# Optimization experiments

Measured on AMD Instinct MI355X. Metric: run time of the kernel, lower is better.

## Reference

```python
import jax, jax.numpy as jnp
import numpy as np

B, S, E, H = 4, 1024, 1024, 16
HD = E // H  # 64


def setup_inputs() -> dict:
    key = jax.random.key(0)
    ks = jax.random.split(key, 9)
    scale = 1.0 / np.sqrt(E)
    x = jax.random.normal(ks[0], (B, S, E), dtype=jnp.float32)
    attention_mask = jnp.ones((B, S, S), dtype=jnp.int32)
    # per-head projection weights, batched over heads: [H, E, HD]
    Wq = jax.random.normal(ks[1], (H, E, HD), dtype=jnp.float32) * scale
    Wk = jax.random.normal(ks[2], (H, E, HD), dtype=jnp.float32) * scale
    Wv = jax.random.normal(ks[3], (H, E, HD), dtype=jnp.float32) * scale
    bq = jax.random.normal(ks[4], (H, HD), dtype=jnp.float32) * scale
    bk = jax.random.normal(ks[5], (H, HD), dtype=jnp.float32) * scale
    bv = jax.random.normal(ks[6], (H, HD), dtype=jnp.float32) * scale
    # output projection, torch Linear convention: [out_features, in_features]
    Wo = jax.random.normal(ks[7], (E, E), dtype=jnp.float32) * scale
    bo = jax.random.normal(ks[8], (E,), dtype=jnp.float32) * scale
    return {"x": x, "attention_mask": attention_mask, "Wq": Wq, "bq": bq,
            "Wk": Wk, "bk": bk, "Wv": Wv, "bv": bv, "Wo": Wo, "bo": bo}


def reference(x, attention_mask, Wq, bq, Wk, bk, Wv, bv, Wo, bo):
    # batched-over-heads QKV projections: (B,S,E) x (H,E,HD) -> (B,H,S,HD)
    q = jnp.einsum('bse,hed->bhsd', x, Wq) + bq[None, :, None, :]
    k = jnp.einsum('bse,hed->bhsd', x, Wk) + bk[None, :, None, :]
    v = jnp.einsum('bse,hed->bhsd', x, Wv) + bv[None, :, None, :]
    scores = jnp.einsum('bhsd,bhtd->bhst', q, k) / jnp.sqrt(jnp.float32(HD))
    mask = attention_mask[:, None, :, :]  # (B,1,S,S) broadcast over heads
    scores = jnp.where(mask == 0, -jnp.inf, scores)
    weights = jax.nn.softmax(scores, axis=-1)
    out = jnp.einsum('bhst,bhtd->bhsd', weights, v)
    # concat heads on last dim: (B,S,H*HD) == (B,S,E)
    out = out.transpose(0, 2, 1, 3).reshape(B, S, E)
    return out @ Wo.T + bo
```

## Files before the change

### kernel.cpp

```cpp
#include <hip/hip_runtime.h>
#include <hip/hip_bf16.h>

#define NB 4
#define SEQ 1024
#define EMB 1024
#define NH 16
#define HD 64

typedef unsigned short u16;
typedef __attribute__((ext_vector_type(8))) __bf16 bf16x8;
typedef __attribute__((ext_vector_type(8))) short short8;
typedef __attribute__((ext_vector_type(4))) float floatx4;

__device__ inline u16 f2b_rn(float f) {
    union { float f; unsigned int i; } x; x.f = f;
    unsigned int r = (x.i + 0x7FFFu + ((x.i >> 16) & 1u)) >> 16;
    return (u16)r;
}
__device__ inline bf16x8 s2b(short8 v) {
    union { short8 s; bf16x8 b; } x; x.s = v; return x.b;
}

__device__ inline void gload_lds16(const void* g, void* l) {
    __builtin_amdgcn_global_load_lds(
        (const __attribute__((address_space(1))) void*)g,
        (__attribute__((address_space(3))) void*)l, 16, 0, 0);
}

__device__ inline bf16x8 ldsfrag(const u16* base, int r, int c) {
    return s2b(*(const short8*)&base[r * 64 + (c ^ ((r & 7) * 8))]);
}

__device__ inline void cvt8(const float* __restrict__ s, u16* __restrict__ d) {
    float4 a = *(const float4*)(s);
    float4 b = *(const float4*)(s + 4);
    union { u16 u[8]; int4 v; } o;
    o.u[0] = f2b_rn(a.x); o.u[1] = f2b_rn(a.y); o.u[2] = f2b_rn(a.z); o.u[3] = f2b_rn(a.w);
    o.u[4] = f2b_rn(b.x); o.u[5] = f2b_rn(b.y); o.u[6] = f2b_rn(b.z); o.u[7] = f2b_rn(b.w);
    *(int4*)(d) = o.v;
}

__global__ __launch_bounds__(256) void prep(
    const float* __restrict__ x, const float* __restrict__ Wq,
    const float* __restrict__ Wk, const float* __restrict__ Wv,
    const float* __restrict__ Wo, const int* __restrict__ mask,
    u16* __restrict__ xb, u16* __restrict__ Wt, u16* __restrict__ Wob,
    unsigned long long* __restrict__ bits)
{
    __shared__ u16 T[64 * 80];
    int bx = blockIdx.x;
    int tid = threadIdx.x;

    if (bx < 2048) {
        int i = bx * 2048 + tid * 8;
        cvt8(x + i, xb + i);
    } else if (bx < 2560) {
        int i = (bx - 2048) * 2048 + tid * 8;
        cvt8(Wo + i, Wob + i);
    } else if (bx < 3328) {
        int bx2 = bx - 2560;
        int e0 = (bx2 & 15) * 64;
        int ph = bx2 >> 4;
        int p = ph >> 4, h = ph & 15;
        const float* W = (p == 0 ? Wq : (p == 1 ? Wk : Wv)) + h * (EMB * HD);
        #pragma unroll
        for (int c = 0; c < 2; ++c) {
            int flat = c * 2048 + tid * 8;
            int r = flat >> 6;
            int d = flat & 63;
            cvt8(W + (size_t)(e0 + r) * HD + d, &T[r * 80 + d]);
        }
        __syncthreads();
        int d = tid >> 2;
        int ec = tid & 3;
        union { u16 u[16]; int4 v[2]; } tmp;
        #pragma unroll
        for (int i = 0; i < 16; ++i) tmp.u[i] = T[(ec * 16 + i) * 80 + d];
        u16* dst = Wt + ((size_t)(p * NH + h) * HD + d) * EMB + e0 + ec * 16;
        *(int4*)(dst) = tmp.v[0];
        *(int4*)(dst + 8) = tmp.v[1];
    } else {
        int gw = (bx - 3328) * 4 + (tid >> 6);
        int lane = tid & 63;
        int m = mask[(size_t)gw * 64 + lane];
        unsigned long long bl = __ballot(m != 0);
        if (lane == 0) bits[gw] = bl;
    }
}

__global__ __launch_bounds__(256) void qkv_gemm(
    const u16* __restrict__ x,
    const u16* __restrict__ Wt2,
    const float* __restrict__ bq, const float* __restrict__ bk, const float* __restrict__ bv,
    u16* __restrict__ Q, u16* __restrict__ K, u16* __restrict__ Vt)
{
    __shared__ u16 As[128 * 64];
    __shared__ u16 Bs[128 * 64];

    int m0 = blockIdx.x * 128;
    int n0 = blockIdx.y * 128;
    int tid = threadIdx.x;
    int w = tid >> 6, lane = tid & 63, quad = lane >> 4, ln = lane & 15;
    int wm = w & 1, wn = w >> 1;

    floatx4 acc[4][4] = {};

    for (int k0 = 0; k0 < EMB; k0 += 64) {
        __syncthreads();
        #pragma unroll
        for (int i = 0; i < 4; ++i) {
            int flat0 = i * 256 + (tid & 192);
            int flat = flat0 + lane;
            int r = flat >> 3;
            int c = ((flat & 7) ^ (r & 7)) * 8;
            gload_lds16(x   + (size_t)(m0 + r) * EMB + k0 + c, As + flat0 * 8);
            gload_lds16(Wt2 + (size_t)(n0 + r) * EMB + k0 + c, Bs + flat0 * 8);
        }
        __syncthreads();

        #pragma unroll
        for (int kk = 0; kk < 2; ++kk) {
            bf16x8 a[4], bf[4];
            #pragma unroll
            for (int mt = 0; mt < 4; ++mt)
                a[mt] = ldsfrag(As, wm * 64 + mt * 16 + ln, kk * 32 + quad * 8);
            #pragma unroll
            for (int nc = 0; nc < 4; ++nc)
                bf[nc] = ldsfrag(Bs, wn * 64 + nc * 16 + ln, kk * 32 + quad * 8);
            #pragma unroll
            for (int mt = 0; mt < 4; ++mt)
                #pragma unroll
                for (int nc = 0; nc < 4; ++nc)
                    acc[mt][nc] = __builtin_amdgcn_mfma_f32_16x16x32_bf16(a[mt], bf[nc], acc[mt][nc], 0, 0, 0);
        }
    }

    int p = n0 >> 10;
    const float* bias = (p == 0 ? bq : (p == 1 ? bk : bv));
    if (p < 2) {
        u16* Out = (p == 0) ? Q : K;
        float qs = (p == 0) ? 0.125f * 1.44269504f : 1.0f;
        #pragma unroll
        for (int nc = 0; nc < 4; ++nc) {
            int n = n0 + wn * 64 + nc * 16 + ln;
            int h = (n >> 6) & 15, d = n & 63;
            float bv_ = bias[n & 1023];
            #pragma unroll
            for (int mt = 0; mt < 4; ++mt) {
                #pragma unroll
                for (int reg = 0; reg < 4; ++reg) {
                    int m = m0 + wm * 64 + mt * 16 + quad * 4 + reg;
                    int b_ = m >> 10, s = m & 1023;
                    Out[((size_t)(b_ * NH + h) * SEQ + s) * HD + d] = f2b_rn((acc[mt][nc][reg] + bv_) * qs);
                }
            }
        }
    } else {
        #pragma unroll
        for (int nc = 0; nc < 4; ++nc) {
            int n = n0 + wn * 64 + nc * 16 + ln;
            int h = (n >> 6) & 15, d = n & 63;
            float bv_ = bias[n & 1023];
            #pragma unroll
            for (int mt = 0; mt < 4; ++mt) {
                int m = m0 + wm * 64 + mt * 16 + quad * 4;
                int b_ = m >> 10, s = m & 1023;
                union { u16 u[4]; uint2 v; } pk;
                #pragma unroll
                for (int reg = 0; reg < 4; ++reg)
                    pk.u[reg] = f2b_rn(acc[mt][nc][reg] + bv_);
                *(uint2*)&Vt[((size_t)(b_ * NH + h) * HD + d) * SEQ + s] = pk.v;
            }
        }
    }
}

__global__ __launch_bounds__(128) void attn(
    const u16* __restrict__ Q, const u16* __restrict__ K, const u16* __restrict__ Vt,
    const unsigned long long* __restrict__ bits,
    u16* __restrict__ Aout)
{
    const int PP = 72;
    __shared__ u16 Ks[64 * 64];
    __shared__ u16 Vs[80 * 64];
    __shared__ u16 Ps[64 * PP];

    int q0 = blockIdx.x * 64;
    int bh = blockIdx.y;
    int b = bh >> 4, h = bh & 15;
    const u16* Qb = Q  + (size_t)bh * SEQ * HD;
    const u16* Kb = K  + (size_t)bh * SEQ * HD;
    const u16* Vb = Vt + (size_t)bh * HD * SEQ;

    int tid = threadIdx.x;
    int w = tid >> 6, lane = tid & 63, quad = lane >> 4, ln = lane & 15;

    if (tid < 16) *(uint2*)&Vs[64 * 64 + tid * 4] = make_uint2(0x3F803F80u, 0x3F803F80u);

    bf16x8 qf[2][2];
    #pragma unroll
    for (int s = 0; s < 2; ++s) {
        const u16* qp = Qb + (size_t)(q0 + w * 32 + s * 16 + ln) * HD + quad * 8;
        union { int4 i; bf16x8 b; } c0, c1;
        c0.i = *(const int4*)(qp);
        c1.i = *(const int4*)(qp + 32);
        qf[s][0] = c0.b; qf[s][1] = c1.b;
    }

    floatx4 o[2][5] = {};

    for (int tt = 0; tt < SEQ / 64; ++tt) {
        int t0 = tt * 64;
        __syncthreads();
        #pragma unroll
        for (int i = 0; i < 4; ++i) {
            int flat0 = i * 128 + (tid & 64);
            int flat = flat0 + lane;
            int r = flat >> 3;
            int c = ((flat & 7) ^ (r & 7)) * 8;
            gload_lds16(Kb + (size_t)(t0 + r) * HD + c, Ks + flat0 * 8);
            gload_lds16(Vb + (size_t)r * SEQ + t0 + c, Vs + flat0 * 8);
        }
        __syncthreads();

        floatx4 sc[2][4] = {};
        #pragma unroll
        for (int kk = 0; kk < 2; ++kk) {
            bf16x8 kf[4];
            #pragma unroll
            for (int tb = 0; tb < 4; ++tb)
                kf[tb] = ldsfrag(Ks, tb * 16 + ln, kk * 32 + quad * 8);
            #pragma unroll
            for (int s = 0; s < 2; ++s)
                #pragma unroll
                for (int tb = 0; tb < 4; ++tb)
                    sc[s][tb] = __builtin_amdgcn_mfma_f32_16x16x32_bf16(kf[tb], qf[s][kk], sc[s][tb], 0, 0, 0);
        }

        #pragma unroll
        for (int s = 0; s < 2; ++s) {
            unsigned long long bm = bits[((size_t)b * SEQ + q0 + w * 32 + s * 16 + ln) * 16 + tt];
            if (__any(bm != ~0ull)) {
                #pragma unroll
                for (int tb = 0; tb < 4; ++tb)
                    #pragma unroll
                    for (int reg = 0; reg < 4; ++reg)
                        if (!((bm >> (tb * 16 + quad * 4 + reg)) & 1)) sc[s][tb][reg] = -1e30f;
            }
        }

        #pragma unroll
        for (int s = 0; s < 2; ++s) {
            int mrow = w * 32 + s * 16 + ln;
            #pragma unroll
            for (int tb = 0; tb < 4; ++tb) {
                union { float f; unsigned int i; } e0_, e1_, e2_, e3_;
                e0_.f = __builtin_amdgcn_exp2f(sc[s][tb][0]);
                e1_.f = __builtin_amdgcn_exp2f(sc[s][tb][1]);
                e2_.f = __builtin_amdgcn_exp2f(sc[s][tb][2]);
                e3_.f = __builtin_amdgcn_exp2f(sc[s][tb][3]);
                uint2 pk;
                pk.x = ((e0_.i + 0x8000u) >> 16) | ((e1_.i + 0x8000u) & 0xFFFF0000u);
                pk.y = ((e2_.i + 0x8000u) >> 16) | ((e3_.i + 0x8000u) & 0xFFFF0000u);
                *(uint2*)&Ps[mrow * PP + tb * 16 + quad * 4] = pk;
            }
        }

        #pragma unroll
        for (int kk = 0; kk < 2; ++kk) {
            bf16x8 vf[5];
            #pragma unroll
            for (int dt = 0; dt < 5; ++dt)
                vf[dt] = ldsfrag(Vs, dt * 16 + ln, kk * 32 + quad * 8);
            #pragma unroll
            for (int s = 0; s < 2; ++s) {
                bf16x8 pf = s2b(*(const short8*)&Ps[(w * 32 + s * 16 + ln) * PP + kk * 32 + quad * 8]);
                #pragma unroll
                for (int dt = 0; dt < 5; ++dt)
                    o[s][dt] = __builtin_amdgcn_mfma_f32_16x16x32_bf16(pf, vf[dt], o[s][dt], 0, 0, 0);
            }
        }
    }

    #pragma unroll
    for (int s = 0; s < 2; ++s) {
        #pragma unroll
        for (int reg = 0; reg < 4; ++reg) {
            float l = __shfl(o[s][4][reg], lane & 48, 64);
            float inv = 1.0f / l;
            int m = q0 + w * 32 + s * 16 + quad * 4 + reg;
            #pragma unroll
            for (int dt = 0; dt < 4; ++dt)
                Aout[((size_t)b * SEQ + m) * EMB + h * HD + dt * 16 + ln] = f2b_rn(o[s][dt][reg] * inv);
        }
    }
}

__global__ __launch_bounds__(256) void out_proj(
    const u16* __restrict__ A,
    const u16* __restrict__ Wo,
    const float* __restrict__ bo,
    float* __restrict__ Out)
{
    __shared__ u16 As[128 * 64];
    __shared__ u16 Bs[128 * 64];

    int m0 = blockIdx.x * 128;
    int n0 = blockIdx.y * 128;
    int tid = threadIdx.x;
    int w = tid >> 6, lane = tid & 63, quad = lane >> 4, ln = lane & 15;
    int wm = w & 1, wn = w >> 1;

    floatx4 acc[4][4] = {};

    for (int k0 = 0; k0 < EMB; k0 += 64) {
        __syncthreads();
        #pragma unroll
        for (int i = 0; i < 4; ++i) {
            int flat0 = i * 256 + (tid & 192);
            int flat = flat0 + lane;
            int r = flat >> 3;
            int c = ((flat & 7) ^ (r & 7)) * 8;
            gload_lds16(A  + (size_t)(m0 + r) * EMB + k0 + c, As + flat0 * 8);
            gload_lds16(Wo + (size_t)(n0 + r) * EMB + k0 + c, Bs + flat0 * 8);
        }
        __syncthreads();

        #pragma unroll
        for (int kk = 0; kk < 2; ++kk) {
            bf16x8 a[4], bf[4];
            #pragma unroll
            for (int mt = 0; mt < 4; ++mt)
                a[mt] = ldsfrag(As, wm * 64 + mt * 16 + ln, kk * 32 + quad * 8);
            #pragma unroll
            for (int nc = 0; nc < 4; ++nc)
                bf[nc] = ldsfrag(Bs, wn * 64 + nc * 16 + ln, kk * 32 + quad * 8);
            #pragma unroll
            for (int mt = 0; mt < 4; ++mt)
                #pragma unroll
                for (int nc = 0; nc < 4; ++nc)
                    acc[mt][nc] = __builtin_amdgcn_mfma_f32_16x16x32_bf16(a[mt], bf[nc], acc[mt][nc], 0, 0, 0);
        }
    }

    #pragma unroll
    for (int nc = 0; nc < 4; ++nc) {
        int n = n0 + wn * 64 + nc * 16 + ln;
        float bb = bo[n];
        #pragma unroll
        for (int mt = 0; mt < 4; ++mt) {
            #pragma unroll
            for (int reg = 0; reg < 4; ++reg) {
                int m = m0 + wm * 64 + mt * 16 + quad * 4 + reg;
                Out[(size_t)m * EMB + n] = acc[mt][nc][reg] + bb;
            }
        }
    }
}

extern "C" void kernel_launch(void* const* d_in, const int* in_sizes, int n_in,
                              void* d_out, int out_size, void* d_ws, size_t ws_size,
                              hipStream_t stream) {
    const float* x  = (const float*)d_in[0];
    const int*   mk = (const int*)d_in[1];
    const float* Wq = (const float*)d_in[2];
    const float* bq = (const float*)d_in[3];
    const float* Wk = (const float*)d_in[4];
    const float* bk = (const float*)d_in[5];
    const float* Wv = (const float*)d_in[6];
    const float* bv = (const float*)d_in[7];
    const float* Wo = (const float*)d_in[8];
    const float* bo = (const float*)d_in[9];
    float* out = (float*)d_out;

    const size_t MB = 1u << 20;
    char* ws = (char*)d_ws;
    u16* xb  = (u16*)ws;
    u16* Wt  = (u16*)(ws + 8 * MB);
    u16* Wob = (u16*)(ws + 14 * MB);
    unsigned long long* bits = (unsigned long long*)(ws + 16 * MB);
    u16* Qw  = (u16*)(ws + 16 * MB + 512 * 1024);
    u16* Kw  = (u16*)(ws + 24 * MB + 512 * 1024);
    u16* Vtw = (u16*)(ws + 32 * MB + 512 * 1024);
    u16* Ao  = xb;

    prep<<<19712, 256, 0, stream>>>(x, Wq, Wk, Wv, Wo, mk, xb, Wt, Wob, bits);
    qkv_gemm<<<dim3((NB * SEQ) / 128, 3 * EMB / 128), 256, 0, stream>>>(
        xb, Wt, bq, bk, bv, Qw, Kw, Vtw);
    attn<<<dim3(SEQ / 64, NB * NH), 128, 0, stream>>>(Qw, Kw, Vtw, bits, Ao);
    out_proj<<<dim3((NB * SEQ) / 128, EMB / 128), 256, 0, stream>>>(Ao, Wob, bo, out);
}
```

Before: 207.7 us.

## Rebalance work across prep, attention and output projection kernels

The mask-to-bitmask pass now has each wave process 16 rows, which cuts the prep grid size. Attention blocks go from 2 to 4 waves, each owning 16 query rows instead of 32. This lowers per-thread registers and splits K/V tile loading across more threads. The output projection halves its M tile to 64, doubling the grid to give better CU coverage at the cost of more B-tile reloads per output.

```diff
diff --git a/kernel.cpp b/kernel.cpp
--- a/kernel.cpp
+++ b/kernel.cpp
@@ -80,11 +80,15 @@
         *(int4*)(dst) = tmp.v[0];
         *(int4*)(dst + 8) = tmp.v[1];
     } else {
-        int gw = (bx - 3328) * 4 + (tid >> 6);
+        int base = (bx - 3328) * 64 + (tid >> 6) * 16;
         int lane = tid & 63;
-        int m = mask[(size_t)gw * 64 + lane];
-        unsigned long long bl = __ballot(m != 0);
-        if (lane == 0) bits[gw] = bl;
+        #pragma unroll
+        for (int i = 0; i < 16; ++i) {
+            int gw = base + i;
+            int m = mask[(size_t)gw * 64 + lane];
+            unsigned long long bl = __ballot(m != 0);
+            if (lane == 0) bits[gw] = bl;
+        }
     }
 }
 
@@ -175,14 +179,14 @@
     }
 }
 
-__global__ __launch_bounds__(128) void attn(
+__global__ __launch_bounds__(256) void attn(
     const u16* __restrict__ Q, const u16* __restrict__ K, const u16* __restrict__ Vt,
     const unsigned long long* __restrict__ bits,
     u16* __restrict__ Aout)
 {
     const int PP = 72;
     __shared__ u16 Ks[64 * 64];
-    __shared__ u16 Vs[80 * 64];
+    __shared__ u16 Vs[72 * 64];
     __shared__ u16 Ps[64 * PP];
 
     int q0 = blockIdx.x * 64;
@@ -197,24 +201,24 @@
 
     if (tid < 16) *(uint2*)&Vs[64 * 64 + tid * 4] = make_uint2(0x3F803F80u, 0x3F803F80u);
 
-    bf16x8 qf[2][2];
-    #pragma unroll
-    for (int s = 0; s < 2; ++s) {
-        const u16* qp = Qb + (size_t)(q0 + w * 32 + s * 16 + ln) * HD + quad * 8;
+    bf16x8 qf[2];
+    {
+        const u16* qp = Qb + (size_t)(q0 + w * 16 + ln) * HD + quad * 8;
         union { int4 i; bf16x8 b; } c0, c1;
         c0.i = *(const int4*)(qp);
         c1.i = *(const int4*)(qp + 32);
-        qf[s][0] = c0.b; qf[s][1] = c1.b;
-    }
-
-    floatx4 o[2][5] = {};
+        qf[0] = c0.b; qf[1] = c1.b;
+    }
+    const unsigned long long* brow = bits + ((size_t)b * SEQ + q0 + w * 16 + ln) * 16;
+
+    floatx4 o[5] = {};
 
     for (int tt = 0; tt < SEQ / 64; ++tt) {
         int t0 = tt * 64;
         __syncthreads();
         #pragma unroll
-        for (int i = 0; i < 4; ++i) {
-            int flat0 = i * 128 + (tid & 64);
+        for (int i = 0; i < 2; ++i) {
+            int flat0 = i * 256 + (tid & 192);
             int flat = flat0 + lane;
             int r = flat >> 3;
             int c = ((flat & 7) ^ (r & 7)) * 8;
@@ -223,42 +227,35 @@
         }
         __syncthreads();
 
-        floatx4 sc[2][4] = {};
+        floatx4 sc[4] = {};
         #pragma unroll
         for (int kk = 0; kk < 2; ++kk) {
-            bf16x8 kf[4];
             #pragma unroll
             for (int tb = 0; tb < 4; ++tb)
-                kf[tb] = ldsfrag(Ks, tb * 16 + ln, kk * 32 + quad * 8);
-            #pragma unroll
-            for (int s = 0; s < 2; ++s)
-                #pragma unroll
-                for (int tb = 0; tb < 4; ++tb)
-                    sc[s][tb] = __builtin_amdgcn_mfma_f32_16x16x32_bf16(kf[tb], qf[s][kk], sc[s][tb], 0, 0, 0);
-        }
-
-        #pragma unroll
-        for (int s = 0; s < 2; ++s) {
-            unsigned long long bm = bits[((size_t)b * SEQ + q0 + w * 32 + s * 16 + ln) * 16 + tt];
+                sc[tb] = __builtin_amdgcn_mfma_f32_16x16x32_bf16(
+                    ldsfrag(Ks, tb * 16 + ln, kk * 32 + quad * 8), qf[kk], sc[tb], 0, 0, 0);
+        }
+
+        {
+            unsigned long long bm = brow[tt];
             if (__any(bm != ~0ull)) {
                 #pragma unroll
                 for (int tb = 0; tb < 4; ++tb)
                     #pragma unroll
                     for (int reg = 0; reg < 4; ++reg)
-                        if (!((bm >> (tb * 16 + quad * 4 + reg)) & 1)) sc[s][tb][reg] = -1e30f;
-            }
-        }
-
-        #pragma unroll
-        for (int s = 0; s < 2; ++s) {
-            int mrow = w * 32 + s * 16 + ln;
+                        if (!((bm >> (tb * 16 + quad * 4 + reg)) & 1)) sc[tb][reg] = -1e30f;
+            }
+        }
+
+        {
+            int mrow = w * 16 + ln;
             #pragma unroll
             for (int tb = 0; tb < 4; ++tb) {
                 union { float f; unsigned int i; } e0_, e1_, e2_, e3_;
-                e0_.f = __builtin_amdgcn_exp2f(sc[s][tb][0]);
-                e1_.f = __builtin_amdgcn_exp2f(sc[s][tb][1]);
-                e2_.f = __builtin_amdgcn_exp2f(sc[s][tb][2]);
-                e3_.f = __builtin_amdgcn_exp2f(sc[s][tb][3]);
+                e0_.f = __builtin_amdgcn_exp2f(sc[tb][0]);
+                e1_.f = __builtin_amdgcn_exp2f(sc[tb][1]);
+                e2_.f = __builtin_amdgcn_exp2f(sc[tb][2]);
+                e3_.f = __builtin_amdgcn_exp2f(sc[tb][3]);
                 uint2 pk;
                 pk.x = ((e0_.i + 0x8000u) >> 16) | ((e1_.i + 0x8000u) & 0xFFFF0000u);
                 pk.y = ((e2_.i + 0x8000u) >> 16) | ((e3_.i + 0x8000u) & 0xFFFF0000u);
@@ -268,31 +265,22 @@
 
         #pragma unroll
         for (int kk = 0; kk < 2; ++kk) {
-            bf16x8 vf[5];
+            bf16x8 pf = s2b(*(const short8*)&Ps[(w * 16 + ln) * PP + kk * 32 + quad * 8]);
             #pragma unroll
             for (int dt = 0; dt < 5; ++dt)
-                vf[dt] = ldsfrag(Vs, dt * 16 + ln, kk * 32 + quad * 8);
-            #pragma unroll
-            for (int s = 0; s < 2; ++s) {
-                bf16x8 pf = s2b(*(const short8*)&Ps[(w * 32 + s * 16 + ln) * PP + kk * 32 + quad * 8]);
-                #pragma unroll
-                for (int dt = 0; dt < 5; ++dt)
-                    o[s][dt] = __builtin_amdgcn_mfma_f32_16x16x32_bf16(pf, vf[dt], o[s][dt], 0, 0, 0);
-            }
+                o[dt] = __builtin_amdgcn_mfma_f32_16x16x32_bf16(
+                    pf, ldsfrag(Vs, dt * 16 + ln, kk * 32 + quad * 8), o[dt], 0, 0, 0);
         }
     }
 
     #pragma unroll
-    for (int s = 0; s < 2; ++s) {
-        #pragma unroll
-        for (int reg = 0; reg < 4; ++reg) {
-            float l = __shfl(o[s][4][reg], lane & 48, 64);
-            float inv = 1.0f / l;
-            int m = q0 + w * 32 + s * 16 + quad * 4 + reg;
-            #pragma unroll
-            for (int dt = 0; dt < 4; ++dt)
-                Aout[((size_t)b * SEQ + m) * EMB + h * HD + dt * 16 + ln] = f2b_rn(o[s][dt][reg] * inv);
-        }
+    for (int reg = 0; reg < 4; ++reg) {
+        float l = __shfl(o[4][reg], lane & 48, 64);
+        float inv = 1.0f / l;
+        int m = q0 + w * 16 + quad * 4 + reg;
+        #pragma unroll
+        for (int dt = 0; dt < 4; ++dt)
+            Aout[((size_t)b * SEQ + m) * EMB + h * HD + dt * 16 + ln] = f2b_rn(o[dt][reg] * inv);
     }
 }
 
@@ -302,44 +290,51 @@
     const float* __restrict__ bo,
     float* __restrict__ Out)
 {
-    __shared__ u16 As[128 * 64];
+    __shared__ u16 As[64 * 64];
     __shared__ u16 Bs[128 * 64];
 
-    int m0 = blockIdx.x * 128;
+    int m0 = blockIdx.x * 64;
     int n0 = blockIdx.y * 128;
     int tid = threadIdx.x;
     int w = tid >> 6, lane = tid & 63, quad = lane >> 4, ln = lane & 15;
     int wm = w & 1, wn = w >> 1;
 
-    floatx4 acc[4][4] = {};
+    floatx4 acc[2][4] = {};
 
     for (int k0 = 0; k0 < EMB; k0 += 64) {
         __syncthreads();
+        #pragma unroll
+        for (int i = 0; i < 2; ++i) {
+            int flat0 = i * 256 + (tid & 192);
+            int flat = flat0 + lane;
+            int r = flat >> 3;
+            int c = ((flat & 7) ^ (r & 7)) * 8;
+            gload_lds16(A + (size_t)(m0 + r) * EMB + k0 + c, As + flat0 * 8);
+        }
         #pragma unroll
         for (int i = 0; i < 4; ++i) {
             int flat0 = i * 256 + (tid & 192);
             int flat = flat0 + lane;
             int r = flat >> 3;
             int c = ((flat & 7) ^ (r & 7)) * 8;
-            gload_lds16(A  + (size_t)(m0 + r) * EMB + k0 + c, As + flat0 * 8);
             gload_lds16(Wo + (size_t)(n0 + r) * EMB + k0 + c, Bs + flat0 * 8);
         }
         __syncthreads();
 
         #pragma unroll
         for (int kk = 0; kk < 2; ++kk) {
-            bf16x8 a[4], bf[4];
-            #pragma unroll
-            for (int mt = 0; mt < 4; ++mt)
-                a[mt] = ldsfrag(As, wm * 64 + mt * 16 + ln, kk * 32 + quad * 8);
+            bf16x8 a[2], bfr[4];
+            #pragma unroll
+            for (int mt = 0; mt < 2; ++mt)
+                a[mt] = ldsfrag(As, wm * 32 + mt * 16 + ln, kk * 32 + quad * 8);
             #pragma unroll
             for (int nc = 0; nc < 4; ++nc)
-                bf[nc] = ldsfrag(Bs, wn * 64 + nc * 16 + ln, kk * 32 + quad * 8);
-            #pragma unroll
-            for (int mt = 0; mt < 4; ++mt)
+                bfr[nc] = ldsfrag(Bs, wn * 64 + nc * 16 + ln, kk * 32 + quad * 8);
+            #pragma unroll
+            for (int mt = 0; mt < 2; ++mt)
                 #pragma unroll
                 for (int nc = 0; nc < 4; ++nc)
-                    acc[mt][nc] = __builtin_amdgcn_mfma_f32_16x16x32_bf16(a[mt], bf[nc], acc[mt][nc], 0, 0, 0);
+                    acc[mt][nc] = __builtin_amdgcn_mfma_f32_16x16x32_bf16(a[mt], bfr[nc], acc[mt][nc], 0, 0, 0);
         }
     }
 
@@ -348,10 +343,10 @@
         int n = n0 + wn * 64 + nc * 16 + ln;
         float bb = bo[n];
         #pragma unroll
-        for (int mt = 0; mt < 4; ++mt) {
+        for (int mt = 0; mt < 2; ++mt) {
             #pragma unroll
             for (int reg = 0; reg < 4; ++reg) {
-                int m = m0 + wm * 64 + mt * 16 + quad * 4 + reg;
+                int m = m0 + wm * 32 + mt * 16 + quad * 4 + reg;
                 Out[(size_t)m * EMB + n] = acc[mt][nc][reg] + bb;
             }
         }
@@ -384,9 +379,9 @@
     u16* Vtw = (u16*)(ws + 32 * MB + 512 * 1024);
     u16* Ao  = xb;
 
-    prep<<<19712, 256, 0, stream>>>(x, Wq, Wk, Wv, Wo, mk, xb, Wt, Wob, bits);
+    prep<<<4352, 256, 0, stream>>>(x, Wq, Wk, Wv, Wo, mk, xb, Wt, Wob, bits);
     qkv_gemm<<<dim3((NB * SEQ) / 128, 3 * EMB / 128), 256, 0, stream>>>(
         xb, Wt, bq, bk, bv, Qw, Kw, Vtw);
-    attn<<<dim3(SEQ / 64, NB * NH), 128, 0, stream>>>(Qw, Kw, Vtw, bits, Ao);
-    out_proj<<<dim3((NB * SEQ) / 128, EMB / 128), 256, 0, stream>>>(Ao, Wob, bo, out);
-}
+    attn<<<dim3(SEQ / 64, NB * NH), 256, 0, stream>>>(Qw, Kw, Vtw, bits, Ao);
+    out_proj<<<dim3((NB * SEQ) / 64, EMB / 128), 256, 0, stream>>>(Ao, Wob, bo, out);
+}
```

New measurement: 214.3 us. 1.03x slower.
